# Performance work log

Measured on AMD Instinct MI355X. Metric: run time of the kernel, lower is better.

Reference implementation:

```python
import jax, jax.numpy as jnp
import numpy as np

# Module config (from init_kwargs)
KH, KW = 3, 3          # kernel_size
SH, SW = 2, 2          # stride
PH, PW = 1, 1          # padding
EPS = 1e-8             # temperature clamp eps
DEN_EPS = 1e-12        # denominator stabilizer (hardcoded in kornia)
DN = ('NCHW', 'OIHW', 'NCHW')


def _window_grid_kernel(kh, kw):
    # window coordinates residual to window center, normalized to [-1, 1]
    ys, xs = jnp.meshgrid(jnp.arange(kh, dtype=jnp.float32),
                          jnp.arange(kw, dtype=jnp.float32), indexing='ij')
    gx = xs * (2.0 / (kw - 1)) - 1.0
    gy = ys * (2.0 / (kh - 1)) - 1.0
    return jnp.stack([gx, gy], axis=0)[:, None]  # (2,1,kh,kw), ch0=x, ch1=y


def _center_kernel(kh, kw):
    k = jnp.zeros((2, 2, kh, kw), jnp.float32)
    k = k.at[0, 0, kh // 2, kw // 2].set(1.0)
    k = k.at[1, 1, kh // 2, kw // 2].set(1.0)
    return k  # (2,2,kh,kw)


def _sum_pool(x):
    # pool_coef * avg_pool2d(count_include_pad=True) == windowed sum with zero pad
    return jax.lax.reduce_window(x, 0.0, jax.lax.add,
                                 (1, 1, KH, KW), (1, 1, SH, SW),
                                 [(0, 0), (0, 0), (PH, PH), (PW, PW)])


def setup_inputs() -> dict:
    key = jax.random.key(0)
    x = jax.random.normal(key, (8, 16, 512, 512), dtype=jnp.float32)
    temperature = jnp.ones((), dtype=jnp.float32)
    return {"x": x, "temperature": temperature}


def reference(x, temperature):
    b, c, h, w = x.shape
    xf = x.reshape(b * c, 1, h, w)

    x_exp = jnp.exp(xf / jnp.maximum(temperature, EPS))

    den = _sum_pool(x_exp) + DEN_EPS                     # (BC,1,Ho,Wo)
    resp_maxima = _sum_pool(x_exp * xf) / den            # softmax-pooled values

    # weighted sum of window-relative coordinates
    coords_num = jax.lax.conv_general_dilated(
        x_exp, _window_grid_kernel(KH, KW), (SH, SW),
        [(PH, PH), (PW, PW)], dimension_numbers=DN)      # (BC,2,Ho,Wo)

    # global grid (x, y) pixel coordinates, center-picked per window
    ys, xs = jnp.meshgrid(jnp.arange(h, dtype=jnp.float32),
                          jnp.arange(w, dtype=jnp.float32), indexing='ij')
    grid_global = jnp.stack([xs, ys], axis=0)[None]      # (1,2,h,w)
    grid_pooled = jax.lax.conv_general_dilated(
        grid_global, _center_kernel(KH, KW), (SH, SW),
        [(PH, PH), (PW, PW)], dimension_numbers=DN)      # (1,2,Ho,Wo)

    coords_max = coords_num / den + grid_pooled          # broadcast over BC

    # normalized_coordinates=True: map pixel coords to [-1, 1]
    cx = coords_max[:, 0] * (2.0 / (w - 1)) - 1.0
    cy = coords_max[:, 1] * (2.0 / (h - 1)) - 1.0
    coords_max = jnp.stack([cx, cy], axis=1)             # (BC,2,Ho,Wo)

    return coords_max, resp_maxima
```

## Files before the change

### kernel.cpp

```cpp
#include <hip/hip_runtime.h>


#define H  512
#define W  512
#define HO 256
#define WO 256
#define BC 128

__global__ __launch_bounds__(256) void casm_kernel(
    const float* __restrict__ x, const float* __restrict__ temp,
    float* __restrict__ out)
{
    int idx = blockIdx.x * 256 + threadIdx.x;
    int wo = idx & (WO - 1);
    int ho = (idx >> 8) & (HO - 1);
    int bc = idx >> 16;

    float invT = 1.0f / fmaxf(temp[0], 1e-8f);

    const float* __restrict__ xp = x + (size_t)bc * (H * W);
    int r0 = 2 * ho - 1;
    int c0 = 2 * wo - 1;

    float den = 1e-12f;
    float num_v = 0.f, num_gx = 0.f, num_gy = 0.f;

#pragma unroll
    for (int kh = 0; kh < 3; ++kh) {
        int r = r0 + kh;
        if (r < 0) continue;
        const float* __restrict__ row = xp + r * W;
#pragma unroll
        for (int kw = 0; kw < 3; ++kw) {
            int c = c0 + kw;
            if (c < 0) continue;
            float v = row[c];
            float e = expf(v * invT);
            den    += e;
            num_v  += e * v;
            num_gx += e * (float)(kw - 1);
            num_gy += e * (float)(kh - 1);
        }
    }

    float inv_den = 1.0f / den;
    const float scale = 2.0f / 511.0f;
    float cx   = (num_gx * inv_den + (float)(2 * wo)) * scale - 1.0f;
    float cy   = (num_gy * inv_den + (float)(2 * ho)) * scale - 1.0f;
    float resp = num_v * inv_den;

    size_t pix   = (size_t)ho * WO + wo;
    size_t cbase = (size_t)bc * (2 * HO * WO) + pix;
    out[cbase]            = cx;
    out[cbase + HO * WO]  = cy;
    out[(size_t)BC * 2 * HO * WO + (size_t)bc * HO * WO + pix] = resp;
}

extern "C" void kernel_launch(void* const* d_in, const int* in_sizes, int n_in,
                              void* d_out, int out_size, void* d_ws, size_t ws_size,
                              hipStream_t stream) {
    const float* x    = (const float*)d_in[0];
    const float* temp = (const float*)d_in[1];
    float* out        = (float*)d_out;

    int total  = BC * HO * WO;
    int blocks = total / 256;
    casm_kernel<<<blocks, 256, 0, stream>>>(x, temp, out);
}
```

Measured before the change: 244.3 us.

## Compute four outputs per thread with vectorized loads and shared exponentials

Each thread now processes four adjacent output columns, loading a row segment with two float4 loads plus one halo element. Each exponential is computed once and reused by the overlapping windows, and results are written with float4 stores. expf and division are replaced with the hardware exp2 and reciprocal intrinsics, which may slightly change precision. The aim is to cut redundant transcendental work and the number of memory instructions.

```diff
diff --git a/kernel.cpp b/kernel.cpp
--- a/kernel.cpp
+++ b/kernel.cpp
@@ -7,53 +7,77 @@
 #define WO 256
 #define BC 128
 
+struct Acc { float den, numv, gx, gy; };
+
+__device__ __forceinline__ void do_row(const float* __restrict__ row, int t,
+                                       float mL, float k, float rs, Acc* a)
+{
+    float v[9];
+    v[0] = row[t ? 8 * t - 1 : 0];
+    float4 q1 = *(const float4*)(row + 8 * t);
+    float4 q2 = *(const float4*)(row + 8 * t + 4);
+    v[1] = q1.x; v[2] = q1.y; v[3] = q1.z; v[4] = q1.w;
+    v[5] = q2.x; v[6] = q2.y; v[7] = q2.z; v[8] = q2.w;
+
+    float e[9];
+#pragma unroll
+    for (int i = 0; i < 9; ++i) e[i] = __builtin_amdgcn_exp2f(k * v[i]);
+    e[0] *= mL;
+
+#pragma unroll
+    for (int j = 0; j < 4; ++j) {
+        float e0 = e[2 * j], e1 = e[2 * j + 1], e2 = e[2 * j + 2];
+        float rsum = e0 + e1 + e2;
+        a[j].den += rsum;
+        a[j].gy   = fmaf(rs, rsum, a[j].gy);
+        a[j].gx  += e2 - e0;
+        a[j].numv = fmaf(e0, v[2 * j],
+                    fmaf(e1, v[2 * j + 1],
+                    fmaf(e2, v[2 * j + 2], a[j].numv)));
+    }
+}
+
 __global__ __launch_bounds__(256) void casm_kernel(
     const float* __restrict__ x, const float* __restrict__ temp,
     float* __restrict__ out)
 {
     int idx = blockIdx.x * 256 + threadIdx.x;
-    int wo = idx & (WO - 1);
-    int ho = (idx >> 8) & (HO - 1);
-    int bc = idx >> 16;
+    int t  = idx & 63;
+    int ho = (idx >> 6) & (HO - 1);
+    int bc = idx >> 14;
 
-    float invT = 1.0f / fmaxf(temp[0], 1e-8f);
+    float k = 1.44269504088896340736f / fmaxf(temp[0], 1e-8f);
+    float mL = t ? 1.0f : 0.0f;
 
     const float* __restrict__ xp = x + (size_t)bc * (H * W);
     int r0 = 2 * ho - 1;
-    int c0 = 2 * wo - 1;
 
-    float den = 1e-12f;
-    float num_v = 0.f, num_gx = 0.f, num_gy = 0.f;
+    Acc a[4];
+#pragma unroll
+    for (int j = 0; j < 4; ++j) { a[j].den = 1e-12f; a[j].numv = 0.f; a[j].gx = 0.f; a[j].gy = 0.f; }
 
+    if (r0 >= 0)
+        do_row(xp + r0 * W,       t, mL, k, -1.0f, a);
+    do_row(xp + (r0 + 1) * W,     t, mL, k,  0.0f, a);
+    do_row(xp + (r0 + 2) * W,     t, mL, k,  1.0f, a);
+
+    const float scale = 2.0f / 511.0f;
+    float4 cx4, cy4, rp4;
+    float* cxp = &cx4.x; float* cyp = &cy4.x; float* rpp = &rp4.x;
 #pragma unroll
-    for (int kh = 0; kh < 3; ++kh) {
-        int r = r0 + kh;
-        if (r < 0) continue;
-        const float* __restrict__ row = xp + r * W;
-#pragma unroll
-        for (int kw = 0; kw < 3; ++kw) {
-            int c = c0 + kw;
-            if (c < 0) continue;
-            float v = row[c];
-            float e = expf(v * invT);
-            den    += e;
-            num_v  += e * v;
-            num_gx += e * (float)(kw - 1);
-            num_gy += e * (float)(kh - 1);
-        }
+    for (int j = 0; j < 4; ++j) {
+        float inv_den = __builtin_amdgcn_rcpf(a[j].den);
+        int wo = 4 * t + j;
+        cxp[j] = (a[j].gx * inv_den + (float)(2 * wo)) * scale - 1.0f;
+        cyp[j] = (a[j].gy * inv_den + (float)(2 * ho)) * scale - 1.0f;
+        rpp[j] = a[j].numv * inv_den;
     }
 
-    float inv_den = 1.0f / den;
-    const float scale = 2.0f / 511.0f;
-    float cx   = (num_gx * inv_den + (float)(2 * wo)) * scale - 1.0f;
-    float cy   = (num_gy * inv_den + (float)(2 * ho)) * scale - 1.0f;
-    float resp = num_v * inv_den;
-
-    size_t pix   = (size_t)ho * WO + wo;
+    size_t pix   = (size_t)ho * WO + 4 * t;
     size_t cbase = (size_t)bc * (2 * HO * WO) + pix;
-    out[cbase]            = cx;
-    out[cbase + HO * WO]  = cy;
-    out[(size_t)BC * 2 * HO * WO + (size_t)bc * HO * WO + pix] = resp;
+    *(float4*)(out + cbase)            = cx4;
+    *(float4*)(out + cbase + HO * WO)  = cy4;
+    *(float4*)(out + (size_t)BC * 2 * HO * WO + (size_t)bc * HO * WO + pix) = rp4;
 }
 
 extern "C" void kernel_launch(void* const* d_in, const int* in_sizes, int n_in,
@@ -63,7 +87,7 @@
     const float* temp = (const float*)d_in[1];
     float* out        = (float*)d_out;
 
-    int total  = BC * HO * WO;
+    int total  = BC * HO * (WO / 4);
     int blocks = total / 256;
     casm_kernel<<<blocks, 256, 0, stream>>>(x, temp, out);
 }
```

Measured after the change: 219.8 us. 1.11x faster.

## Stage input rows in LDS with even/odd split and compute four outputs per thread

Applied to the files above, without the earlier changes.

Each block now loads a 9-row strip of one channel into shared memory with 128-bit loads, deinterleaving even and odd columns. Each thread then produces four adjacent outputs from vectorized LDS reads. The exp2 intrinsic replaces expf, and a fast reciprocal is used. Results are written with vector stores. This removes redundant global loads and repeated exponentials of overlapping window elements, at the cost of LDS traffic, a barrier, and -1e4 sentinel padding that stands in for excluded border elements.

```diff
diff --git a/kernel.cpp b/kernel.cpp
--- a/kernel.cpp
+++ b/kernel.cpp
@@ -7,53 +7,103 @@
 #define WO 256
 #define BC 128
 
+typedef float f32x4 __attribute__((ext_vector_type(4)));
+
+#define ROWSTRIDE 520
+
 __global__ __launch_bounds__(256) void casm_kernel(
     const float* __restrict__ x, const float* __restrict__ temp,
     float* __restrict__ out)
 {
-    int idx = blockIdx.x * 256 + threadIdx.x;
-    int wo = idx & (WO - 1);
-    int ho = (idx >> 8) & (HO - 1);
-    int bc = idx >> 16;
+    __shared__ float lds[9 * ROWSTRIDE];
 
-    float invT = 1.0f / fmaxf(temp[0], 1e-8f);
+    int tid = threadIdx.x;
+    int hq  = blockIdx.x & 63;
+    int bc  = blockIdx.x >> 6;
+
+    float k = 1.44269504088896340736f / fmaxf(temp[0], 1e-8f);
 
     const float* __restrict__ xp = x + (size_t)bc * (H * W);
-    int r0 = 2 * ho - 1;
-    int c0 = 2 * wo - 1;
-
-    float den = 1e-12f;
-    float num_v = 0.f, num_gx = 0.f, num_gy = 0.f;
+    int r0 = 8 * hq - 1;
 
 #pragma unroll
-    for (int kh = 0; kh < 3; ++kh) {
-        int r = r0 + kh;
-        if (r < 0) continue;
-        const float* __restrict__ row = xp + r * W;
+    for (int p = 0; p < 3; ++p) {
+        int chunk = tid + p * 256;
+        if (chunk < 576) {
+            int rr = chunk >> 6, c8 = chunk & 63;
+            int r = r0 + rr;
+            f32x4 q1, q2;
+            if (r >= 0) {
+                const float* row = xp + r * W + 8 * c8;
+                q1 = *(const f32x4*)row;
+                q2 = *(const f32x4*)(row + 4);
+            } else {
+                q1 = q2 = (f32x4)(-1e4f);
+            }
+            f32x4 ev = {q1.x, q1.z, q2.x, q2.z};
+            f32x4 od = {q1.y, q1.w, q2.y, q2.w};
+            *(f32x4*)&lds[rr * ROWSTRIDE + 4 * c8]       = ev;
+            *(f32x4*)&lds[rr * ROWSTRIDE + 260 + 4 * c8] = od;
+        }
+    }
+    if (tid < 9) lds[tid * ROWSTRIDE + 259] = -1e4f;
+    __syncthreads();
+
+    int t  = tid & 63;
+    int oh = tid >> 6;
+    int ho = 4 * hq + oh;
+
+    float den[4] = {1e-12f, 1e-12f, 1e-12f, 1e-12f};
+    float numv[4] = {0.f, 0.f, 0.f, 0.f};
+    float gx[4] = {0.f, 0.f, 0.f, 0.f};
+    float gy[4] = {0.f, 0.f, 0.f, 0.f};
+
 #pragma unroll
-        for (int kw = 0; kw < 3; ++kw) {
-            int c = c0 + kw;
-            if (c < 0) continue;
-            float v = row[c];
-            float e = expf(v * invT);
-            den    += e;
-            num_v  += e * v;
-            num_gx += e * (float)(kw - 1);
-            num_gy += e * (float)(kh - 1);
+    for (int dr = 0; dr < 3; ++dr) {
+        int rbase = (2 * oh + dr) * ROWSTRIDE;
+        float rs = (float)(dr - 1);
+        f32x4 ev = *(const f32x4*)&lds[rbase + 4 * t];
+        f32x4 od = *(const f32x4*)&lds[rbase + 260 + 4 * t];
+        float om = lds[rbase + 259 + 4 * t];
+
+        float em = __builtin_amdgcn_exp2f(k * om);
+        f32x4 ee, eo;
+#pragma unroll
+        for (int j = 0; j < 4; ++j) {
+            ee[j] = __builtin_amdgcn_exp2f(k * ev[j]);
+            eo[j] = __builtin_amdgcn_exp2f(k * od[j]);
+        }
+#pragma unroll
+        for (int j = 0; j < 4; ++j) {
+            float e0 = j ? eo[j - 1] : em;
+            float v0 = j ? od[j - 1] : om;
+            float e1 = ee[j], v1 = ev[j];
+            float e2 = eo[j], v2 = od[j];
+            float rsum = e0 + e1 + e2;
+            den[j] += rsum;
+            gy[j]   = fmaf(rs, rsum, gy[j]);
+            gx[j]  += e2 - e0;
+            numv[j] = fmaf(e0, v0, fmaf(e1, v1, fmaf(e2, v2, numv[j])));
         }
     }
 
-    float inv_den = 1.0f / den;
     const float scale = 2.0f / 511.0f;
-    float cx   = (num_gx * inv_den + (float)(2 * wo)) * scale - 1.0f;
-    float cy   = (num_gy * inv_den + (float)(2 * ho)) * scale - 1.0f;
-    float resp = num_v * inv_den;
+    f32x4 cx4, cy4, rp4;
+#pragma unroll
+    for (int j = 0; j < 4; ++j) {
+        float inv_den = __builtin_amdgcn_rcpf(den[j]);
+        int wo = 4 * t + j;
+        cx4[j] = (gx[j] * inv_den + (float)(2 * wo)) * scale - 1.0f;
+        cy4[j] = (gy[j] * inv_den + (float)(2 * ho)) * scale - 1.0f;
+        rp4[j] = numv[j] * inv_den;
+    }
 
-    size_t pix   = (size_t)ho * WO + wo;
-    size_t cbase = (size_t)bc * (2 * HO * WO) + pix;
-    out[cbase]            = cx;
-    out[cbase + HO * WO]  = cy;
-    out[(size_t)BC * 2 * HO * WO + (size_t)bc * HO * WO + pix] = resp;
+    size_t cstride = (size_t)HO * WO;
+    size_t pix     = (size_t)ho * WO + 4 * t;
+    size_t cbase   = (size_t)bc * (2 * cstride) + pix;
+    *(f32x4*)(out + cbase)           = cx4;
+    *(f32x4*)(out + cbase + cstride) = cy4;
+    *(f32x4*)(out + (size_t)BC * 2 * cstride + (size_t)bc * cstride + pix) = rp4;
 }
 
 extern "C" void kernel_launch(void* const* d_in, const int* in_sizes, int n_in,
@@ -63,7 +113,6 @@
     const float* temp = (const float*)d_in[1];
     float* out        = (float*)d_out;
 
-    int total  = BC * HO * WO;
-    int blocks = total / 256;
+    int blocks = BC * (HO / 4);
     casm_kernel<<<blocks, 256, 0, stream>>>(x, temp, out);
 }
```

Result: faster. 221.7 us (-9.2%).
